# Kernel optimization log

Hardware: AMD Instinct MI355X
Metric: run time of the kernel (lower is better)

The kernel has to match this reference:

```python
import jax, jax.numpy as jnp
import numpy as np

K = 3  # num_stacks
T = 2  # num_layers
N_NODES = 30000
N_EDGES = 300000
F_IN = 256
F_HID = 256
F_OUT = 64


def _glorot(key, shape):
    fan_in, fan_out = shape[-2], shape[-1]
    s = jnp.sqrt(6.0 / (fan_in + fan_out))
    return jax.random.uniform(key, shape, jnp.float32, -s, s)


def setup_inputs() -> dict:
    key = jax.random.key(0)
    ks = jax.random.split(key, 12)
    x = jax.random.normal(ks[0], (N_NODES, F_IN), jnp.float32)
    edge_index = jax.random.randint(ks[1], (2, N_EDGES), 0, N_NODES, jnp.int64)
    return {
        "x": x,
        "edge_index": edge_index,
        # conv1 (in -> hidden), shared weights across layers
        "init_w1": _glorot(ks[2], (K, F_IN, F_HID)),
        "w1": _glorot(ks[3], (K, F_HID, F_HID)),
        "root_w1": _glorot(ks[4], (K, F_IN, F_HID)),
        "bias1": jnp.zeros((K, 1, F_HID), jnp.float32),
        # conv2 (hidden -> out)
        "init_w2": _glorot(ks[5], (K, F_HID, F_OUT)),
        "w2": _glorot(ks[6], (K, F_OUT, F_OUT)),
        "root_w2": _glorot(ks[7], (K, F_HID, F_OUT)),
        "bias2": jnp.zeros((K, 1, F_OUT), jnp.float32),
    }


def _gcn_norm(edge_index, num_nodes):
    # gcn_norm with add_self_loops=False: deg over destination (col)
    row, col = edge_index[0], edge_index[1]
    deg = jax.ops.segment_sum(jnp.ones((edge_index.shape[1],), jnp.float32), col,
                              num_segments=num_nodes)
    dis = jnp.where(deg > 0, jax.lax.rsqrt(jnp.maximum(deg, 1.0)), 0.0)
    return dis[row] * dis[col]


def _propagate(h, row, col, norm, num_nodes):
    # h: [K, N, F] -> sum over incoming edges of norm * h[src]
    msg = norm[None, :, None] * h[:, row]  # [K, E, F]
    return jax.vmap(lambda m: jax.ops.segment_sum(m, col, num_segments=num_nodes))(msg)


def _arma_conv(x, row, col, norm, init_w, w, root_w, bias, act):
    # shared_weights=True: weight/root_weight reused for every layer t>0 / t
    num_nodes = x.shape[0]
    root = jnp.einsum('nf,kfo->kno', x, root_w) + bias  # [K, N, F_out]
    h = jnp.einsum('nf,kfo->kno', x, init_w)
    for t in range(T):
        if t > 0:
            h = jnp.einsum('kno,kop->knp', h, w)
        h = _propagate(h, row, col, norm, num_nodes)
        h = act(h + root)
    return h.mean(axis=0)  # mean over stacks -> [N, F_out]


def reference(x, edge_index, init_w1, w1, root_w1, bias1, init_w2, w2, root_w2, bias2):
    # eval mode: all dropouts are identity
    row, col = edge_index[0], edge_index[1]
    norm = _gcn_norm(edge_index, x.shape[0])
    h = _arma_conv(x, row, col, norm, init_w1, w1, root_w1, bias1, jax.nn.relu)
    h = jax.nn.relu(h)
    h = _arma_conv(h, row, col, norm, init_w2, w2, root_w2, bias2, lambda t: t)
    return jax.nn.log_softmax(h, axis=1)
```

## Files before the change

kernel.cpp:

```cpp
#include <hip/hip_runtime.h>
#include <hip/hip_bf16.h>

#define NN 30000
#define NE 300000

typedef unsigned short u16;
typedef unsigned int u32;
typedef unsigned long long u64;
typedef short s16x8 __attribute__((ext_vector_type(8)));
typedef float f32x4 __attribute__((ext_vector_type(4)));

__device__ __forceinline__ float bf2f(u16 u) { return __uint_as_float(((u32)u) << 16); }
__device__ __forceinline__ u16 f2bf(float f) {
    u32 u = __float_as_uint(f);
    u32 r = (u + 0x7FFFu + ((u >> 16) & 1u)) >> 16;
    return (u16)r;
}

__global__ void hist_kernel(const int* __restrict__ col, int* __restrict__ deg) {
    int e = blockIdx.x * blockDim.x + threadIdx.x;
    if (e < NE) atomicAdd(&deg[col[e]], 1);
}

__global__ void dis_kernel(const int* __restrict__ deg, float* __restrict__ dis) {
    int i = blockIdx.x * blockDim.x + threadIdx.x;
    if (i < NN) {
        int d = deg[i];
        dis[i] = d > 0 ? rsqrtf((float)d) : 0.0f;
    }
}

__global__ __launch_bounds__(1024) void scan_kernel(const int* __restrict__ deg,
                                                    int* __restrict__ rowptr) {
    __shared__ int buf[1024];
    __shared__ int carry_s;
    if (threadIdx.x == 0) { carry_s = 0; rowptr[0] = 0; }
    __syncthreads();
    for (int base = 0; base < NN; base += 1024) {
        int i = base + (int)threadIdx.x;
        int v = (i < NN) ? deg[i] : 0;
        buf[threadIdx.x] = v;
        __syncthreads();
        for (int off = 1; off < 1024; off <<= 1) {
            int t = (threadIdx.x >= (unsigned)off) ? buf[threadIdx.x - off] : 0;
            __syncthreads();
            buf[threadIdx.x] += t;
            __syncthreads();
        }
        int carry = carry_s;
        if (i < NN) rowptr[i + 1] = carry + buf[threadIdx.x];
        __syncthreads();
        if (threadIdx.x == 1023) carry_s = carry + buf[1023];
        __syncthreads();
    }
}

__global__ void scatter_kernel(const int* __restrict__ row, const int* __restrict__ col,
                               const int* __restrict__ rowptr, int* __restrict__ cursor,
                               const float* __restrict__ dis, int* __restrict__ src,
                               float* __restrict__ ew) {
    int e = blockIdx.x * blockDim.x + threadIdx.x;
    if (e < NE) {
        int c = col[e];
        int r = row[e];
        int pos = rowptr[c] + atomicAdd(&cursor[c], 1);
        src[pos] = r;
        ew[pos] = dis[r] * dis[c];
    }
}

__global__ void f2bf_vec(const float* __restrict__ in, u16* __restrict__ out, long n4) {
    long i = (long)blockIdx.x * blockDim.x + threadIdx.x;
    if (i < n4) {
        float4 v = *(const float4*)&in[i * 4];
        u16 o[4] = { f2bf(v.x), f2bf(v.y), f2bf(v.z), f2bf(v.w) };
        *(u64*)&out[i * 4] = *(u64*)o;
    }
}

__global__ void prep_w(const float* __restrict__ W, u16* __restrict__ Wt, int Kd, int Od) {
    long idx = (long)blockIdx.x * blockDim.x + threadIdx.x;
    long total = 3L * Kd * Od;
    if (idx < total) {
        int kk = idx % Kd;
        long rest = idx / Kd;
        int o = rest % Od;
        int k = rest / Od;
        Wt[idx] = f2bf(W[((long)k * Kd + kk) * Od + o]);
    }
}

template<int U64W>
__global__ __launch_bounds__(U64W < 64 ? 64 : U64W) void prop_node(
    const u16* __restrict__ h, u16* __restrict__ out,
    const int* __restrict__ rowptr, const int* __restrict__ src,
    const float* __restrict__ ew)
{
    int n = blockIdx.x;
    int t = threadIdx.x;
    if (U64W < 64 && t >= U64W) return;
    int beg = rowptr[n], end = rowptr[n + 1];
    const u64* hu = (const u64*)h;
    float a0 = 0.f, a1 = 0.f, a2 = 0.f, a3 = 0.f;
    int e = beg;
    int s = 0; float w = 0.f;
    if (e < end) { s = src[e]; w = ew[e]; }
    while (e < end) {
        int e2 = e + 1; int s2 = 0; float w2 = 0.f;
        if (e2 < end) { s2 = src[e2]; w2 = ew[e2]; }
        u64 v = hu[(size_t)s * U64W + t];
        a0 += w * bf2f((u16)v);
        a1 += w * bf2f((u16)(v >> 16));
        a2 += w * bf2f((u16)(v >> 32));
        a3 += w * bf2f((u16)(v >> 48));
        e = e2; s = s2; w = w2;
    }
    u16 o[4] = { f2bf(a0), f2bf(a1), f2bf(a2), f2bf(a3) };
    ((u64*)out)[(size_t)n * U64W + t] = *(u64*)o;
}

template<int BN, int HAS_ADD, int HAS_BIAS, int RELU>
__global__ __launch_bounds__(256) void gemm_one(
    const u16* __restrict__ A, int pitchA, int stOffA,
    const u16* __restrict__ Wt, const float* __restrict__ bias,
    const u16* __restrict__ addend, u16* __restrict__ out,
    int M, int O, int K, int NY)
{
    constexpr int NJ = BN / 32;
    constexpr int NB = (BN * 4) / 256;
    const int nyz = NY * 3;
    const int yz = blockIdx.x % nyz;
    const int mb = blockIdx.x / nyz;
    const int m0 = mb * 128;
    const int o0 = (yz % NY) * BN;
    const int st = yz / NY;
    const u16* Ak = A + (size_t)st * stOffA;
    const u16* Wk = Wt + (size_t)st * O * K;
    __shared__ u16 As[128][40];
    __shared__ u16 Bs[BN][40];
    const int tid = threadIdx.x;
    const int lane = tid & 63, wave = tid >> 6;
    const int wrow = wave >> 1, wcol = wave & 1;
    const int l15 = lane & 15, l4 = lane >> 4;
    f32x4 acc[4][NJ] = {};
    for (int kt = 0; kt < K; kt += 32) {
#pragma unroll
        for (int hh = 0; hh < 2; hh++) {
            int c = tid + hh * 256;
            int row = c >> 2, kc = (c & 3) * 8;
            int gr = m0 + row;
            uint4 v = {0, 0, 0, 0};
            if (gr < M) v = *(const uint4*)&Ak[(size_t)gr * pitchA + kt + kc];
            *(uint4*)&As[row][kc] = v;
        }
#pragma unroll
        for (int hh = 0; hh < NB; hh++) {
            int c = tid + hh * 256;
            int row = c >> 2, kc = (c & 3) * 8;
            *(uint4*)&Bs[row][kc] = *(const uint4*)&Wk[(size_t)(o0 + row) * K + kt + kc];
        }
        __syncthreads();
        s16x8 bfr[NJ];
#pragma unroll
        for (int j = 0; j < NJ; j++)
            bfr[j] = *(const s16x8*)&Bs[wcol * (BN / 2) + j * 16 + l15][l4 * 8];
#pragma unroll
        for (int i = 0; i < 4; i++) {
            s16x8 a = *(const s16x8*)&As[wrow * 64 + i * 16 + l15][l4 * 8];
#pragma unroll
            for (int j = 0; j < NJ; j++)
                acc[i][j] = __builtin_amdgcn_mfma_f32_16x16x32_bf16(a, bfr[j], acc[i][j], 0, 0, 0);
        }
        __syncthreads();
    }
#pragma unroll
    for (int i = 0; i < 4; i++)
#pragma unroll
        for (int j = 0; j < NJ; j++) {
            int cg = o0 + wcol * (BN / 2) + j * 16 + l15;
            float bv = HAS_BIAS ? bias[st * O + cg] : 0.0f;
#pragma unroll
            for (int q = 0; q < 4; q++) {
                int rg = m0 + wrow * 64 + i * 16 + l4 * 4 + q;
                if (rg < M) {
                    float v = acc[i][j][q] + bv;
                    if (HAS_ADD) v += bf2f(addend[((size_t)rg * 3 + st) * O + cg]);
                    if (RELU) v = fmaxf(v, 0.0f);
                    out[((size_t)rg * 3 + st) * O + cg] = f2bf(v);
                }
            }
        }
}

template<int RELU2>
__global__ __launch_bounds__(256) void gemm_dual(
    const u16* __restrict__ A1, const u16* __restrict__ A2,
    const u16* __restrict__ W1, const u16* __restrict__ W2,
    const float* __restrict__ bias,
    u16* __restrict__ out1, u16* __restrict__ out2,
    int M, int O, int K, int NY)
{
    const int nyz = NY * 3;
    const int yz = blockIdx.x % nyz;
    const int mb = blockIdx.x / nyz;
    const int m0 = mb * 128;
    const int o0 = (yz % NY) * 64;
    const int st = yz / NY;
    const u16* W1k = W1 + (size_t)st * O * K;
    const u16* W2k = W2 + (size_t)st * O * K;
    __shared__ u16 As1[128][40];
    __shared__ u16 As2[128][40];
    __shared__ u16 Bs1[64][40];
    __shared__ u16 Bs2[64][40];
    const int tid = threadIdx.x;
    const int lane = tid & 63, wave = tid >> 6;
    const int wrow = wave >> 1, wcol = wave & 1;
    const int l15 = lane & 15, l4 = lane >> 4;
    const int srow = tid >> 2;
    const int skoff = (tid & 3) * 8;

    f32x4 acc1[4][2] = {};
    f32x4 acc2[4][2] = {};
    for (int kt = 0; kt < K; kt += 32) {
#pragma unroll
        for (int hh = 0; hh < 2; hh++) {
            int c = tid + hh * 256;
            int row = c >> 2, kc = (c & 3) * 8;
            int gr = m0 + row;
            uint4 v1 = {0, 0, 0, 0}, v2 = {0, 0, 0, 0};
            if (gr < M) {
                v1 = *(const uint4*)&A1[(size_t)gr * K + kt + kc];
                v2 = *(const uint4*)&A2[(size_t)gr * K + kt + kc];
            }
            *(uint4*)&As1[row][kc] = v1;
            *(uint4*)&As2[row][kc] = v2;
        }
        *(uint4*)&Bs1[srow][skoff] = *(const uint4*)&W1k[(size_t)(o0 + srow) * K + kt + skoff];
        *(uint4*)&Bs2[srow][skoff] = *(const uint4*)&W2k[(size_t)(o0 + srow) * K + kt + skoff];
        __syncthreads();
        s16x8 b10 = *(const s16x8*)&Bs1[wcol * 32 + l15][l4 * 8];
        s16x8 b11 = *(const s16x8*)&Bs1[wcol * 32 + 16 + l15][l4 * 8];
        s16x8 b20 = *(const s16x8*)&Bs2[wcol * 32 + l15][l4 * 8];
        s16x8 b21 = *(const s16x8*)&Bs2[wcol * 32 + 16 + l15][l4 * 8];
#pragma unroll
        for (int i = 0; i < 4; i++) {
            s16x8 a1 = *(const s16x8*)&As1[wrow * 64 + i * 16 + l15][l4 * 8];
            s16x8 a2 = *(const s16x8*)&As2[wrow * 64 + i * 16 + l15][l4 * 8];
            acc1[i][0] = __builtin_amdgcn_mfma_f32_16x16x32_bf16(a1, b10, acc1[i][0], 0, 0, 0);
            acc1[i][1] = __builtin_amdgcn_mfma_f32_16x16x32_bf16(a1, b11, acc1[i][1], 0, 0, 0);
            acc2[i][0] = __builtin_amdgcn_mfma_f32_16x16x32_bf16(a2, b20, acc2[i][0], 0, 0, 0);
            acc2[i][1] = __builtin_amdgcn_mfma_f32_16x16x32_bf16(a2, b21, acc2[i][1], 0, 0, 0);
        }
        __syncthreads();
    }
#pragma unroll
    for (int j = 0; j < 2; j++) {
        int cg = o0 + wcol * 32 + j * 16 + l15;
        float bv = bias[st * O + cg];
#pragma unroll
        for (int i = 0; i < 4; i++)
#pragma unroll
            for (int q = 0; q < 4; q++) {
                int rg = m0 + wrow * 64 + i * 16 + l4 * 4 + q;
                if (rg < M) {
                    float o1 = acc1[i][j][q] + bv;
                    out1[((size_t)rg * 3 + st) * O + cg] = f2bf(o1);
                    float o2 = acc2[i][j][q] + o1;
                    if (RELU2) o2 = fmaxf(o2, 0.0f);
                    out2[((size_t)rg * 3 + st) * O + cg] = f2bf(o2);
                }
            }
    }
}

__global__ void mean3_256(const u16* __restrict__ h, u16* __restrict__ out) {
    long idx = (long)blockIdx.x * blockDim.x + threadIdx.x;
    const long total = (long)NN * 128;
    if (idx >= total) return;
    long n = idx >> 7; int t = (int)(idx & 127);
    const u32* hu = (const u32*)h;
    u32 a = hu[(n * 3 + 0) * 128 + t], b = hu[(n * 3 + 1) * 128 + t], c = hu[(n * 3 + 2) * 128 + t];
    float lo = (bf2f((u16)a) + bf2f((u16)b) + bf2f((u16)c)) * (1.0f / 3.0f);
    float hi = (bf2f((u16)(a >> 16)) + bf2f((u16)(b >> 16)) + bf2f((u16)(c >> 16))) * (1.0f / 3.0f);
    ((u32*)out)[idx] = (u32)f2bf(lo) | ((u32)f2bf(hi) << 16);
}

__global__ __launch_bounds__(64) void final_ls(const u16* __restrict__ g, float* __restrict__ out) {
    int n = blockIdx.x;
    int f = threadIdx.x;
    long b0 = (long)n * 192 + f;
    float v = (bf2f(g[b0]) + bf2f(g[b0 + 64]) + bf2f(g[b0 + 128])) * (1.0f / 3.0f);
    float m = v;
    for (int off = 32; off; off >>= 1) m = fmaxf(m, __shfl_xor(m, off, 64));
    float s = expf(v - m);
    for (int off = 32; off; off >>= 1) s += __shfl_xor(s, off, 64);
    out[(long)n * 64 + f] = v - m - logf(s);
}

extern "C" void kernel_launch(void* const* d_in, const int* in_sizes, int n_in,
                              void* d_out, int out_size, void* d_ws, size_t ws_size,
                              hipStream_t stream) {
    const float* x = (const float*)d_in[0];
    const int* ei = (const int*)d_in[1];
    const float* init_w1 = (const float*)d_in[2];
    const float* w1 = (const float*)d_in[3];
    const float* root_w1 = (const float*)d_in[4];
    const float* bias1 = (const float*)d_in[5];
    const float* init_w2 = (const float*)d_in[6];
    const float* w2 = (const float*)d_in[7];
    const float* root_w2 = (const float*)d_in[8];
    const float* bias2 = (const float*)d_in[9];
    float* out = (float*)d_out;
    (void)ws_size; (void)n_in; (void)in_sizes; (void)out_size;

    char* ws = (char*)d_ws;
    size_t off = 0;
    auto alloc = [&](size_t bytes) -> void* {
        void* p = ws + off;
        off += (bytes + 255) & ~(size_t)255;
        return p;
    };
    int* deg = (int*)alloc(NN * 4);
    int* rowptr = (int*)alloc((NN + 1) * 4);
    int* cursor = (int*)alloc(NN * 4);
    int* srcb = (int*)alloc((size_t)NE * 4);
    float* ewb = (float*)alloc((size_t)NE * 4);
    float* dis = (float*)alloc(NN * 4);
    u16* iw1t = (u16*)alloc((size_t)3 * 256 * 256 * 2);
    u16* w1t = (u16*)alloc((size_t)3 * 256 * 256 * 2);
    u16* rw1t = (u16*)alloc((size_t)3 * 256 * 256 * 2);
    u16* iw2t = (u16*)alloc((size_t)3 * 64 * 256 * 2);
    u16* rw2t = (u16*)alloc((size_t)3 * 64 * 256 * 2);
    u16* w2t = (u16*)alloc((size_t)3 * 64 * 64 * 2);
    u16* xb = (u16*)alloc((size_t)NN * 256 * 2);
    u16* bufR = (u16*)alloc((size_t)NN * 3 * 256 * 2);
    u16* bufH = (u16*)alloc((size_t)NN * 3 * 256 * 2);
    u16* bufP = (u16*)alloc((size_t)NN * 3 * 256 * 2);
    u16* px = bufP;
    u16* hmean = bufP;
    u16* pm = xb;
    u16* root2 = bufR;
    u16* g1 = bufR + (size_t)3 * NN * 64;
    u16* pg1 = bufR + (size_t)6 * NN * 64;
    u16* g2 = bufR + (size_t)9 * NN * 64;

    const int* e_row = ei;
    const int* e_col = ei + NE;

    hipMemsetAsync(deg, 0, NN * 4, stream);
    hipMemsetAsync(cursor, 0, NN * 4, stream);

    hist_kernel<<<(NE + 255) / 256, 256, 0, stream>>>(e_col, deg);
    dis_kernel<<<(NN + 255) / 256, 256, 0, stream>>>(deg, dis);
    scan_kernel<<<1, 1024, 0, stream>>>(deg, rowptr);
    scatter_kernel<<<(NE + 255) / 256, 256, 0, stream>>>(e_row, e_col, rowptr, cursor, dis, srcb, ewb);

    f2bf_vec<<<(NN * 256 / 4 + 255) / 256, 256, 0, stream>>>(x, xb, (long)NN * 256 / 4);
    prep_w<<<(3 * 256 * 256 + 255) / 256, 256, 0, stream>>>(init_w1, iw1t, 256, 256);
    prep_w<<<(3 * 256 * 256 + 255) / 256, 256, 0, stream>>>(w1, w1t, 256, 256);
    prep_w<<<(3 * 256 * 256 + 255) / 256, 256, 0, stream>>>(root_w1, rw1t, 256, 256);
    prep_w<<<(3 * 64 * 256 + 255) / 256, 256, 0, stream>>>(init_w2, iw2t, 256, 64);
    prep_w<<<(3 * 64 * 256 + 255) / 256, 256, 0, stream>>>(root_w2, rw2t, 256, 64);
    prep_w<<<(3 * 64 * 64 + 255) / 256, 256, 0, stream>>>(w2, w2t, 64, 64);

    const int MB = (NN + 127) / 128;

    prop_node<64><<<NN, 64, 0, stream>>>(xb, px, rowptr, srcb, ewb);
    gemm_dual<1><<<MB * 12, 256, 0, stream>>>(xb, px, rw1t, iw1t, bias1,
                                              bufR, bufH, NN, 256, 256, 4);
    prop_node<192><<<NN, 192, 0, stream>>>(bufH, bufP, rowptr, srcb, ewb);
    gemm_one<128, 1, 0, 1><<<MB * 6, 256, 0, stream>>>(
        bufP, 768, 256, w1t, nullptr, bufR, bufH, NN, 256, 256, 2);
    mean3_256<<<(int)(((long)NN * 128 + 255) / 256), 256, 0, stream>>>(bufH, hmean);

    prop_node<64><<<NN, 64, 0, stream>>>(hmean, pm, rowptr, srcb, ewb);
    gemm_dual<0><<<MB * 3, 256, 0, stream>>>(hmean, pm, rw2t, iw2t, bias2,
                                             root2, g1, NN, 64, 256, 1);
    prop_node<48><<<NN, 64, 0, stream>>>(g1, pg1, rowptr, srcb, ewb);
    gemm_one<64, 1, 0, 0><<<MB * 3, 256, 0, stream>>>(
        pg1, 192, 64, w2t, nullptr, root2, g2, NN, 64, 64, 1);

    final_ls<<<NN, 64, 0, stream>>>(g2, out);
}
```

Baseline: 549.2 us.

## Swap MFMA operands for vectorized epilogue stores and add XCD-aware block remap

The MFMA operand order is swapped in both GEMM kernels so each lane holds four consecutive output columns of one row. The epilogue can then do one 8-byte store, with 8-byte addend and float4 bias loads, instead of four scalar 2-byte stores. It also remaps block IDs so consecutive logical tiles land on the same XCD, which is meant to improve L2 reuse of shared A rows and weights. The remap assumes round-robin dispatch of blocks across 8 XCDs.

```diff
diff --git a/kernel.cpp b/kernel.cpp
--- a/kernel.cpp
+++ b/kernel.cpp
@@ -15,6 +15,14 @@
     u32 u = __float_as_uint(f);
     u32 r = (u + 0x7FFFu + ((u >> 16) & 1u)) >> 16;
     return (u16)r;
+}
+
+__device__ __forceinline__ int xcd_map(int bid, int nwg) {
+    int xcd = bid & 7;
+    int i = bid >> 3;
+    int q = nwg >> 3, r = nwg & 7;
+    int base = (xcd < r) ? xcd * (q + 1) : r * (q + 1) + (xcd - r) * q;
+    return base + i;
 }
 
 __global__ void hist_kernel(const int* __restrict__ col, int* __restrict__ deg) {
@@ -129,8 +137,9 @@
     constexpr int NJ = BN / 32;
     constexpr int NB = (BN * 4) / 256;
     const int nyz = NY * 3;
-    const int yz = blockIdx.x % nyz;
-    const int mb = blockIdx.x / nyz;
+    const int wg = xcd_map(blockIdx.x, gridDim.x);
+    const int yz = wg % nyz;
+    const int mb = wg / nyz;
     const int m0 = mb * 128;
     const int o0 = (yz % NY) * BN;
     const int st = yz / NY;
@@ -169,27 +178,34 @@
             s16x8 a = *(const s16x8*)&As[wrow * 64 + i * 16 + l15][l4 * 8];
 #pragma unroll
             for (int j = 0; j < NJ; j++)
-                acc[i][j] = __builtin_amdgcn_mfma_f32_16x16x32_bf16(a, bfr[j], acc[i][j], 0, 0, 0);
-        }
-        __syncthreads();
-    }
-#pragma unroll
-    for (int i = 0; i < 4; i++)
+                acc[i][j] = __builtin_amdgcn_mfma_f32_16x16x32_bf16(bfr[j], a, acc[i][j], 0, 0, 0);
+        }
+        __syncthreads();
+    }
+#pragma unroll
+    for (int i = 0; i < 4; i++) {
+        int rg = m0 + wrow * 64 + i * 16 + l15;
+        if (rg >= M) continue;
 #pragma unroll
         for (int j = 0; j < NJ; j++) {
-            int cg = o0 + wcol * (BN / 2) + j * 16 + l15;
-            float bv = HAS_BIAS ? bias[st * O + cg] : 0.0f;
+            int cgb = o0 + wcol * (BN / 2) + j * 16 + l4 * 4;
+            size_t ob = ((size_t)rg * 3 + st) * O + cgb;
+            float4 bv = {0.f, 0.f, 0.f, 0.f};
+            if (HAS_BIAS) bv = *(const float4*)&bias[st * O + cgb];
+            u64 av = 0;
+            if (HAS_ADD) av = *(const u64*)&addend[ob];
+            u16 o[4];
 #pragma unroll
             for (int q = 0; q < 4; q++) {
-                int rg = m0 + wrow * 64 + i * 16 + l4 * 4 + q;
-                if (rg < M) {
-                    float v = acc[i][j][q] + bv;
-                    if (HAS_ADD) v += bf2f(addend[((size_t)rg * 3 + st) * O + cg]);
-                    if (RELU) v = fmaxf(v, 0.0f);
-                    out[((size_t)rg * 3 + st) * O + cg] = f2bf(v);
-                }
+                float v = acc[i][j][q];
+                if (HAS_BIAS) v += (&bv.x)[q];
+                if (HAS_ADD) v += bf2f((u16)(av >> (16 * q)));
+                if (RELU) v = fmaxf(v, 0.0f);
+                o[q] = f2bf(v);
             }
-        }
+            *(u64*)&out[ob] = *(u64*)o;
+        }
+    }
 }
 
 template<int RELU2>
@@ -201,8 +217,9 @@
     int M, int O, int K, int NY)
 {
     const int nyz = NY * 3;
-    const int yz = blockIdx.x % nyz;
-    const int mb = blockIdx.x / nyz;
+    const int wg = xcd_map(blockIdx.x, gridDim.x);
+    const int yz = wg % nyz;
+    const int mb = wg / nyz;
     const int m0 = mb * 128;
     const int o0 = (yz % NY) * 64;
     const int st = yz / NY;
@@ -246,30 +263,34 @@
         for (int i = 0; i < 4; i++) {
             s16x8 a1 = *(const s16x8*)&As1[wrow * 64 + i * 16 + l15][l4 * 8];
             s16x8 a2 = *(const s16x8*)&As2[wrow * 64 + i * 16 + l15][l4 * 8];
-            acc1[i][0] = __builtin_amdgcn_mfma_f32_16x16x32_bf16(a1, b10, acc1[i][0], 0, 0, 0);
-            acc1[i][1] = __builtin_amdgcn_mfma_f32_16x16x32_bf16(a1, b11, acc1[i][1], 0, 0, 0);
-            acc2[i][0] = __builtin_amdgcn_mfma_f32_16x16x32_bf16(a2, b20, acc2[i][0], 0, 0, 0);
-            acc2[i][1] = __builtin_amdgcn_mfma_f32_16x16x32_bf16(a2, b21, acc2[i][1], 0, 0, 0);
-        }
-        __syncthreads();
-    }
-#pragma unroll
-    for (int j = 0; j < 2; j++) {
-        int cg = o0 + wcol * 32 + j * 16 + l15;
-        float bv = bias[st * O + cg];
-#pragma unroll
-        for (int i = 0; i < 4; i++)
+            acc1[i][0] = __builtin_amdgcn_mfma_f32_16x16x32_bf16(b10, a1, acc1[i][0], 0, 0, 0);
+            acc1[i][1] = __builtin_amdgcn_mfma_f32_16x16x32_bf16(b11, a1, acc1[i][1], 0, 0, 0);
+            acc2[i][0] = __builtin_amdgcn_mfma_f32_16x16x32_bf16(b20, a2, acc2[i][0], 0, 0, 0);
+            acc2[i][1] = __builtin_amdgcn_mfma_f32_16x16x32_bf16(b21, a2, acc2[i][1], 0, 0, 0);
+        }
+        __syncthreads();
+    }
+#pragma unroll
+    for (int i = 0; i < 4; i++) {
+        int rg = m0 + wrow * 64 + i * 16 + l15;
+        if (rg >= M) continue;
+#pragma unroll
+        for (int j = 0; j < 2; j++) {
+            int cgb = o0 + wcol * 32 + j * 16 + l4 * 4;
+            size_t ob = ((size_t)rg * 3 + st) * O + cgb;
+            float4 bv = *(const float4*)&bias[st * O + cgb];
+            u16 o1[4], o2[4];
 #pragma unroll
             for (int q = 0; q < 4; q++) {
-                int rg = m0 + wrow * 64 + i * 16 + l4 * 4 + q;
-                if (rg < M) {
-                    float o1 = acc1[i][j][q] + bv;
-                    out1[((size_t)rg * 3 + st) * O + cg] = f2bf(o1);
-                    float o2 = acc2[i][j][q] + o1;
-                    if (RELU2) o2 = fmaxf(o2, 0.0f);
-                    out2[((size_t)rg * 3 + st) * O + cg] = f2bf(o2);
-                }
+                float v1 = acc1[i][j][q] + (&bv.x)[q];
+                o1[q] = f2bf(v1);
+                float v2 = acc2[i][j][q] + v1;
+                if (RELU2) v2 = fmaxf(v2, 0.0f);
+                o2[q] = f2bf(v2);
             }
+            *(u64*)&out1[ob] = *(u64*)o1;
+            *(u64*)&out2[ob] = *(u64*)o2;
+        }
     }
 }
 
```

After: 505.4 us. 1.09x faster.
